# Performance work log

Hardware: AMD Instinct MI355X
Metric: run time of the kernel (lower is better)

## Reference

```python
import jax, jax.numpy as jnp
import numpy as np

B, P, K = 2, 8192, 48
C_IN, C_OUT = 64, 64
N_RADIAL = 8
N_SH = 4            # l=0 (1 component) + l=1 (3 components)
NB = N_RADIAL * N_SH
R_MAX = 2.0
SIGMA = R_MAX / N_RADIAL
EPS = 1e-8


def _edge_basis(rel):
    """Per-edge equivariant basis from relative vectors.
    rel: [..., 3] -> basis [..., NB] = radial Gaussians x (Y_00, Y_1m)."""
    d = jnp.linalg.norm(rel, axis=-1)                              # [...]
    centers = jnp.linspace(0.0, R_MAX, N_RADIAL, dtype=rel.dtype)
    radial = jnp.exp(-0.5 * ((d[..., None] - centers) / SIGMA) ** 2)  # [..., R]
    inv = jnp.where(d > EPS, 1.0 / jnp.maximum(d, EPS), 0.0)
    unit = rel * inv[..., None]                                    # [..., 3]
    sh = jnp.concatenate([jnp.ones_like(d)[..., None], unit], -1)  # [..., 4]
    basis = radial[..., :, None] * sh[..., None, :]                # [..., R, 4]
    return basis.reshape(basis.shape[:-2] + (NB,))


def setup_inputs() -> dict:
    key = jax.random.key(0)
    k1, k2, k3, k4, k5 = jax.random.split(key, 5)
    features = jax.random.normal(k1, (B, C_IN, P), dtype=jnp.float32)
    geometry = jax.random.normal(k2, (B, P, 3), dtype=jnp.float32)
    neighbors = jax.random.randint(k3, (B, P, K), 0, P)
    rel_mask = jax.random.uniform(k4, (B, P, K), dtype=jnp.float32)
    # learned kernel weights: [n_basis, c_out, c_in]
    W = jax.random.normal(k5, (NB, C_OUT, C_IN), dtype=jnp.float32) / np.sqrt(NB * C_IN)
    return {"features": features, "geometry": geometry, "neighbors": neighbors,
            "rel_mask": rel_mask, "W": W}


def reference(features, geometry, neighbors, rel_mask, W):
    # gather neighbor positions: [B, P, K, 3]
    nb_geo = jax.vmap(lambda g, n: g[n])(geometry, neighbors)
    rel = nb_geo - geometry[:, :, None, :]                         # relative vectors
    basis = _edge_basis(rel) * rel_mask[..., None]                 # [B, P, K, NB]
    # gather neighbor features: [B, C_in, P, K]
    nb_feat = jax.vmap(lambda f, n: f[:, n])(features, neighbors)
    # per-edge kernel K_e = sum_n basis_n * W[n] applied to neighbor feats,
    # summed over neighbors -- fused into one contraction (never materialize
    # the [B,P,K,C_out,C_in] kernel tensor):
    out = jnp.einsum('bpkn,ncj,bjpk->bcp', basis, W, nb_feat)
    return out
```

## Files before the change

### kernel.cpp

```cpp
#include <hip/hip_runtime.h>
#include <math.h>

#define B_SZ 2
#define P_SZ 8192
#define K_NB 48
#define NRAD 8
#define NJ 2048
#define PTS 8
#define GSTRIDE 2052
#define EPS_D 1e-8f

__global__ __launch_bounds__(256) void k_transpose(const float* __restrict__ f,
                                                   const float* __restrict__ w,
                                                   float* __restrict__ ft,
                                                   float* __restrict__ wt) {
    __shared__ float tile[64][65];
    int blk = blockIdx.x;
    int t = threadIdx.x;
    if (blk < 256) {
        int b = blk >> 7;
        int p0 = (blk & 127) << 6;
        {
            int pp = t & 63, cq = t >> 6;
#pragma unroll
            for (int i = 0; i < 16; ++i) {
                int c = cq * 16 + i;
                tile[c][pp] = f[((size_t)b * 64 + c) * P_SZ + p0 + pp];
            }
        }
        __syncthreads();
        {
            int cc = t & 63, pq = t >> 6;
#pragma unroll
            for (int i = 0; i < 16; ++i) {
                int p = pq * 16 + i;
                ft[((size_t)b * P_SZ + p0 + p) * 64 + cc] = tile[cc][p];
            }
        }
    } else {
        int n = blk - 256;
        {
            int jj = t & 63, cq = t >> 6;
#pragma unroll
            for (int i = 0; i < 16; ++i) {
                int c = cq * 16 + i;
                tile[c][jj] = w[((size_t)n * 64 + c) * 64 + jj];
            }
        }
        __syncthreads();
        {
            int cc = t & 63, jq = t >> 6;
#pragma unroll
            for (int i = 0; i < 16; ++i) {
                int j = jq * 16 + i;
                wt[((size_t)n * 64 + j) * 64 + cc] = tile[cc][j];
            }
        }
    }
}

__global__ __launch_bounds__(512) void k_main(const float* __restrict__ featT,
                                              const float* __restrict__ geometry,
                                              const int* __restrict__ neighbors,
                                              const float* __restrict__ rel_mask,
                                              const float* __restrict__ Wt,
                                              float* __restrict__ out) {
    __shared__ float G[PTS][GSTRIDE];
    __shared__ float sh_l[PTS][K_NB][4];
    __shared__ float d_l[PTS][K_NB];
    __shared__ int   nbrs_l[PTS][K_NB];

    const int t = threadIdx.x;
    const int blk = blockIdx.x;
    const int b = blk >> 10;
    const int pt0 = (blk & 1023) * PTS;

    if (t < PTS * K_NB) {
        int pt = t / K_NB;
        int k = t - pt * K_NB;
        int p = pt0 + pt;
        size_t base = (size_t)b * P_SZ + p;
        int nb = neighbors[base * K_NB + k];
        const float* gp = &geometry[base * 3];
        const float* gn = &geometry[((size_t)b * P_SZ + nb) * 3];
        float rx = gn[0] - gp[0], ry = gn[1] - gp[1], rz = gn[2] - gp[2];
        float d = sqrtf(rx * rx + ry * ry + rz * rz);
        float mask = rel_mask[base * K_NB + k];
        float inv = (d > EPS_D) ? (1.0f / d) : 0.0f;
        sh_l[pt][k][0] = mask;
        sh_l[pt][k][1] = rx * inv * mask;
        sh_l[pt][k][2] = ry * inv * mask;
        sh_l[pt][k][3] = rz * inv * mask;
        d_l[pt][k] = d;
        nbrs_l[pt][k] = nb;
    }
    __syncthreads();

    {
        const int pt = t >> 6;
        const int ng = (t >> 3) & 7;
        const int jg = t & 7;
        const int j0 = jg * 8;
        const float center = (float)ng * (2.0f / 7.0f);
        float acc[4][8];
#pragma unroll
        for (int s = 0; s < 4; ++s)
#pragma unroll
            for (int j = 0; j < 8; ++j) acc[s][j] = 0.0f;

        const float* fbase = featT + (size_t)b * P_SZ * 64;
#pragma unroll 4
        for (int k = 0; k < K_NB; ++k) {
            int nb = nbrs_l[pt][k];
            const float4* fv = (const float4*)(fbase + (size_t)nb * 64 + j0);
            float4 fA = fv[0];
            float4 fB = fv[1];
            float z = (d_l[pt][k] - center) * 4.0f;
            float rad = __expf(-0.5f * z * z);
            float4 s4 = *(const float4*)&sh_l[pt][k][0];
            float bs[4] = {rad * s4.x, rad * s4.y, rad * s4.z, rad * s4.w};
            float fj[8] = {fA.x, fA.y, fA.z, fA.w, fB.x, fB.y, fB.z, fB.w};
#pragma unroll
            for (int s = 0; s < 4; ++s)
#pragma unroll
                for (int j = 0; j < 8; ++j) acc[s][j] += bs[s] * fj[j];
        }
        const int n0 = ng * 4;
#pragma unroll
        for (int s = 0; s < 4; ++s) {
            *(float4*)&G[pt][(n0 + s) * 64 + j0]     = make_float4(acc[s][0], acc[s][1], acc[s][2], acc[s][3]);
            *(float4*)&G[pt][(n0 + s) * 64 + j0 + 4] = make_float4(acc[s][4], acc[s][5], acc[s][6], acc[s][7]);
        }
    }
    __syncthreads();

    float acc2[8][8];
    {
        const int cg = t & 7;
        const int sg = t >> 3;
        const int c0 = cg * 8;
#pragma unroll
        for (int ci = 0; ci < 8; ++ci)
#pragma unroll
            for (int pt = 0; pt < 8; ++pt) acc2[ci][pt] = 0.0f;

        const int njbase = sg * 32;
        const int rot = (sg * 4) & 31;
#pragma unroll
        for (int it = 0; it < 8; ++it) {
            const int njo = njbase + ((it * 4 + rot) & 31);
            float4 g4[8];
#pragma unroll
            for (int pt = 0; pt < 8; ++pt) g4[pt] = *(const float4*)&G[pt][njo];
            float gf[8][4];
#pragma unroll
            for (int pt = 0; pt < 8; ++pt) {
                gf[pt][0] = g4[pt].x; gf[pt][1] = g4[pt].y;
                gf[pt][2] = g4[pt].z; gf[pt][3] = g4[pt].w;
            }
            float wf[4][8];
#pragma unroll
            for (int q = 0; q < 4; ++q) {
                const float4* wp = (const float4*)(Wt + (size_t)(njo + q) * 64 + c0);
                float4 w0 = wp[0], w1 = wp[1];
                wf[q][0] = w0.x; wf[q][1] = w0.y; wf[q][2] = w0.z; wf[q][3] = w0.w;
                wf[q][4] = w1.x; wf[q][5] = w1.y; wf[q][6] = w1.z; wf[q][7] = w1.w;
            }
#pragma unroll
            for (int q = 0; q < 4; ++q)
#pragma unroll
                for (int ci = 0; ci < 8; ++ci)
#pragma unroll
                    for (int pt = 0; pt < 8; ++pt)
                        acc2[ci][pt] += wf[q][ci] * gf[pt][q];
        }

#pragma unroll
        for (int off = 8; off <= 32; off <<= 1)
#pragma unroll
            for (int ci = 0; ci < 8; ++ci)
#pragma unroll
                for (int pt = 0; pt < 8; ++pt)
                    acc2[ci][pt] += __shfl_xor(acc2[ci][pt], off, 64);
    }
    __syncthreads();

    float* partial = &G[0][0];
    if (((t >> 3) & 7) == 0) {
        const int cg = t & 7;
        const int w = t >> 6;
#pragma unroll
        for (int ci = 0; ci < 8; ++ci) {
            int c = cg * 8 + ci;
            int base = w * 552 + c * 8 + cg * 4;
            *(float4*)&partial[base]     = make_float4(acc2[ci][0], acc2[ci][1], acc2[ci][2], acc2[ci][3]);
            *(float4*)&partial[base + 4] = make_float4(acc2[ci][4], acc2[ci][5], acc2[ci][6], acc2[ci][7]);
        }
    }
    __syncthreads();
    {
        const int c = t >> 3, pt = t & 7;
        const int off = c * 8 + (c >> 3) * 4 + pt;
        float s = 0.0f;
#pragma unroll
        for (int w = 0; w < 8; ++w) s += partial[w * 552 + off];
        out[((size_t)b * 64 + c) * P_SZ + pt0 + pt] = s;
    }
}

extern "C" void kernel_launch(void* const* d_in, const int* in_sizes, int n_in,
                              void* d_out, int out_size, void* d_ws, size_t ws_size,
                              hipStream_t stream) {
    const float* features  = (const float*)d_in[0];
    const float* geometry  = (const float*)d_in[1];
    const int*   neighbors = (const int*)d_in[2];
    const float* rel_mask  = (const float*)d_in[3];
    const float* W         = (const float*)d_in[4];
    float* out = (float*)d_out;

    float* featT = (float*)d_ws;
    float* Wt    = (float*)((char*)d_ws + (size_t)B_SZ * P_SZ * 64 * 4);

    k_transpose<<<288, 256, 0, stream>>>(features, W, featT, Wt);
    k_main<<<B_SZ * (P_SZ / PTS), 512, 0, stream>>>(featT, geometry, neighbors,
                                                    rel_mask, Wt, out);
}
```

Baseline: 218.7 us.

## Stage neighbor feature gathers into LDS with double-buffered async global_load_lds

Replaces the per-thread direct global float4 gathers of neighbor features with wave-level global_load_lds transfers into a double-buffered LDS staging area, 8 neighbors per group. The next group is prefetched while the current one is consumed. The aim is to overlap gather latency with the FMA work and to stop the 8 ng-groups in a wave from loading the same feature row redundantly. In exchange it adds about 32KB of LDS on top of the existing ~66KB, which may reduce occupancy. It also relies on manual vmcnt waits with no barrier, which is correct only because each wave reads just its own staging slice.

```diff
diff --git a/kernel.cpp b/kernel.cpp
--- a/kernel.cpp
+++ b/kernel.cpp
@@ -66,6 +66,7 @@
                                               const float* __restrict__ Wt,
                                               float* __restrict__ out) {
     __shared__ float G[PTS][GSTRIDE];
+    __shared__ float fstage[PTS][2][8][64];
     __shared__ float sh_l[PTS][K_NB][4];
     __shared__ float d_l[PTS][K_NB];
     __shared__ int   nbrs_l[PTS][K_NB];
@@ -98,6 +99,7 @@
 
     {
         const int pt = t >> 6;
+        const int lane = t & 63;
         const int ng = (t >> 3) & 7;
         const int jg = t & 7;
         const int j0 = jg * 8;
@@ -109,21 +111,48 @@
             for (int j = 0; j < 8; ++j) acc[s][j] = 0.0f;
 
         const float* fbase = featT + (size_t)b * P_SZ * 64;
-#pragma unroll 4
-        for (int k = 0; k < K_NB; ++k) {
-            int nb = nbrs_l[pt][k];
-            const float4* fv = (const float4*)(fbase + (size_t)nb * 64 + j0);
-            float4 fA = fv[0];
-            float4 fB = fv[1];
-            float z = (d_l[pt][k] - center) * 4.0f;
-            float rad = __expf(-0.5f * z * z);
-            float4 s4 = *(const float4*)&sh_l[pt][k][0];
-            float bs[4] = {rad * s4.x, rad * s4.y, rad * s4.z, rad * s4.w};
-            float fj[8] = {fA.x, fA.y, fA.z, fA.w, fB.x, fB.y, fB.z, fB.w};
-#pragma unroll
-            for (int s = 0; s < 4; ++s)
-#pragma unroll
-                for (int j = 0; j < 8; ++j) acc[s][j] += bs[s] * fj[j];
+        const int esub = lane >> 4;
+        const int coff = (lane & 15) * 4;
+
+        auto stage = [&](int g, int buf) {
+            int e0 = g * 8 + esub;
+            const float* gs0 = fbase + (size_t)nbrs_l[pt][e0] * 64 + coff;
+            __builtin_amdgcn_global_load_lds(
+                (const __attribute__((address_space(1))) unsigned int*)gs0,
+                (__attribute__((address_space(3))) unsigned int*)&fstage[pt][buf][0][0],
+                16, 0, 0);
+            int e1 = e0 + 4;
+            const float* gs1 = fbase + (size_t)nbrs_l[pt][e1] * 64 + coff;
+            __builtin_amdgcn_global_load_lds(
+                (const __attribute__((address_space(1))) unsigned int*)gs1,
+                (__attribute__((address_space(3))) unsigned int*)&fstage[pt][buf][4][0],
+                16, 0, 0);
+        };
+
+        stage(0, 0);
+        for (int g = 0; g < 6; ++g) {
+            const int buf = g & 1;
+            if (g < 5) {
+                stage(g + 1, buf ^ 1);
+                asm volatile("s_waitcnt vmcnt(2)" ::: "memory");
+            } else {
+                asm volatile("s_waitcnt vmcnt(0)" ::: "memory");
+            }
+#pragma unroll
+            for (int ee = 0; ee < 8; ++ee) {
+                const int e = g * 8 + ee;
+                float z = (d_l[pt][e] - center) * 4.0f;
+                float rad = __expf(-0.5f * z * z);
+                float4 s4 = *(const float4*)&sh_l[pt][e][0];
+                float4 fA = *(const float4*)&fstage[pt][buf][ee][j0];
+                float4 fB = *(const float4*)&fstage[pt][buf][ee][j0 + 4];
+                float bs[4] = {rad * s4.x, rad * s4.y, rad * s4.z, rad * s4.w};
+                float fj[8] = {fA.x, fA.y, fA.z, fA.w, fB.x, fB.y, fB.z, fB.w};
+#pragma unroll
+                for (int s = 0; s < 4; ++s)
+#pragma unroll
+                    for (int j = 0; j < 8; ++j) acc[s][j] += bs[s] * fj[j];
+            }
         }
         const int n0 = ng * 4;
 #pragma unroll
```

Result: faster. 210.1 us (-3.9%).

## Double block size to 1024 threads, halving per-thread work in both stages

Applied to the files above, without the earlier changes.

Moves k_main from 512 to 1024 threads per block. Each thread now covers 4 feature channels instead of 8 in the gather stage and 4 output channels instead of 8 in the W contraction, which cuts register pressure and adds waves for hiding gather latency. The cross-wave reduction is rebuilt for 16 waves with a padded stride-9 layout. In exchange there are more redundant basis/exp computations per edge, more shuffles relative to FMAs, and a larger LDS reduction step.

```diff
diff --git a/kernel.cpp b/kernel.cpp
--- a/kernel.cpp
+++ b/kernel.cpp
@@ -59,12 +59,12 @@
     }
 }
 
-__global__ __launch_bounds__(512) void k_main(const float* __restrict__ featT,
-                                              const float* __restrict__ geometry,
-                                              const int* __restrict__ neighbors,
-                                              const float* __restrict__ rel_mask,
-                                              const float* __restrict__ Wt,
-                                              float* __restrict__ out) {
+__global__ __launch_bounds__(1024) void k_main(const float* __restrict__ featT,
+                                               const float* __restrict__ geometry,
+                                               const int* __restrict__ neighbors,
+                                               const float* __restrict__ rel_mask,
+                                               const float* __restrict__ Wt,
+                                               float* __restrict__ out) {
     __shared__ float G[PTS][GSTRIDE];
     __shared__ float sh_l[PTS][K_NB][4];
     __shared__ float d_l[PTS][K_NB];
@@ -97,50 +97,49 @@
     __syncthreads();
 
     {
-        const int pt = t >> 6;
-        const int ng = (t >> 3) & 7;
-        const int jg = t & 7;
-        const int j0 = jg * 8;
+        const int wave = t >> 6;
+        const int lane = t & 63;
+        const int pt = wave >> 1;
+        const int h  = wave & 1;
+        const int ng = lane >> 3;
+        const int jg = lane & 7;
+        const int j0 = h * 32 + jg * 4;
         const float center = (float)ng * (2.0f / 7.0f);
-        float acc[4][8];
+        float acc[4][4];
 #pragma unroll
         for (int s = 0; s < 4; ++s)
 #pragma unroll
-            for (int j = 0; j < 8; ++j) acc[s][j] = 0.0f;
+            for (int j = 0; j < 4; ++j) acc[s][j] = 0.0f;
 
         const float* fbase = featT + (size_t)b * P_SZ * 64;
 #pragma unroll 4
         for (int k = 0; k < K_NB; ++k) {
             int nb = nbrs_l[pt][k];
-            const float4* fv = (const float4*)(fbase + (size_t)nb * 64 + j0);
-            float4 fA = fv[0];
-            float4 fB = fv[1];
+            float4 fv = *(const float4*)(fbase + (size_t)nb * 64 + j0);
             float z = (d_l[pt][k] - center) * 4.0f;
             float rad = __expf(-0.5f * z * z);
             float4 s4 = *(const float4*)&sh_l[pt][k][0];
             float bs[4] = {rad * s4.x, rad * s4.y, rad * s4.z, rad * s4.w};
-            float fj[8] = {fA.x, fA.y, fA.z, fA.w, fB.x, fB.y, fB.z, fB.w};
+            float fj[4] = {fv.x, fv.y, fv.z, fv.w};
 #pragma unroll
             for (int s = 0; s < 4; ++s)
 #pragma unroll
-                for (int j = 0; j < 8; ++j) acc[s][j] += bs[s] * fj[j];
+                for (int j = 0; j < 4; ++j) acc[s][j] += bs[s] * fj[j];
         }
         const int n0 = ng * 4;
 #pragma unroll
-        for (int s = 0; s < 4; ++s) {
-            *(float4*)&G[pt][(n0 + s) * 64 + j0]     = make_float4(acc[s][0], acc[s][1], acc[s][2], acc[s][3]);
-            *(float4*)&G[pt][(n0 + s) * 64 + j0 + 4] = make_float4(acc[s][4], acc[s][5], acc[s][6], acc[s][7]);
-        }
-    }
-    __syncthreads();
-
-    float acc2[8][8];
+        for (int s = 0; s < 4; ++s)
+            *(float4*)&G[pt][(n0 + s) * 64 + j0] = make_float4(acc[s][0], acc[s][1], acc[s][2], acc[s][3]);
+    }
+    __syncthreads();
+
+    float acc2[4][8];
     {
-        const int cg = t & 7;
-        const int sg = t >> 3;
-        const int c0 = cg * 8;
-#pragma unroll
-        for (int ci = 0; ci < 8; ++ci)
+        const int cg = t & 15;
+        const int sg = t >> 4;
+        const int c0 = cg * 4;
+#pragma unroll
+        for (int ci = 0; ci < 4; ++ci)
 #pragma unroll
             for (int pt = 0; pt < 8; ++pt) acc2[ci][pt] = 0.0f;
 
@@ -158,27 +157,25 @@
                 gf[pt][0] = g4[pt].x; gf[pt][1] = g4[pt].y;
                 gf[pt][2] = g4[pt].z; gf[pt][3] = g4[pt].w;
             }
-            float wf[4][8];
+            float wf[4][4];
 #pragma unroll
             for (int q = 0; q < 4; ++q) {
-                const float4* wp = (const float4*)(Wt + (size_t)(njo + q) * 64 + c0);
-                float4 w0 = wp[0], w1 = wp[1];
+                float4 w0 = *(const float4*)(Wt + (size_t)(njo + q) * 64 + c0);
                 wf[q][0] = w0.x; wf[q][1] = w0.y; wf[q][2] = w0.z; wf[q][3] = w0.w;
-                wf[q][4] = w1.x; wf[q][5] = w1.y; wf[q][6] = w1.z; wf[q][7] = w1.w;
             }
 #pragma unroll
             for (int q = 0; q < 4; ++q)
 #pragma unroll
-                for (int ci = 0; ci < 8; ++ci)
+                for (int ci = 0; ci < 4; ++ci)
 #pragma unroll
                     for (int pt = 0; pt < 8; ++pt)
                         acc2[ci][pt] += wf[q][ci] * gf[pt][q];
         }
 
 #pragma unroll
-        for (int off = 8; off <= 32; off <<= 1)
-#pragma unroll
-            for (int ci = 0; ci < 8; ++ci)
+        for (int off = 16; off <= 32; off <<= 1)
+#pragma unroll
+            for (int ci = 0; ci < 4; ++ci)
 #pragma unroll
                 for (int pt = 0; pt < 8; ++pt)
                     acc2[ci][pt] += __shfl_xor(acc2[ci][pt], off, 64);
@@ -186,24 +183,26 @@
     __syncthreads();
 
     float* partial = &G[0][0];
-    if (((t >> 3) & 7) == 0) {
-        const int cg = t & 7;
-        const int w = t >> 6;
-#pragma unroll
-        for (int ci = 0; ci < 8; ++ci) {
-            int c = cg * 8 + ci;
-            int base = w * 552 + c * 8 + cg * 4;
-            *(float4*)&partial[base]     = make_float4(acc2[ci][0], acc2[ci][1], acc2[ci][2], acc2[ci][3]);
-            *(float4*)&partial[base + 4] = make_float4(acc2[ci][4], acc2[ci][5], acc2[ci][6], acc2[ci][7]);
-        }
-    }
-    __syncthreads();
     {
+        const int lane = t & 63;
+        if (lane < 16) {
+            const int w = t >> 6;
+            const int cg = lane;
+#pragma unroll
+            for (int ci = 0; ci < 4; ++ci) {
+                int c = cg * 4 + ci;
+#pragma unroll
+                for (int pt = 0; pt < 8; ++pt)
+                    partial[w * 576 + c * 9 + pt] = acc2[ci][pt];
+            }
+        }
+    }
+    __syncthreads();
+    if (t < 512) {
         const int c = t >> 3, pt = t & 7;
-        const int off = c * 8 + (c >> 3) * 4 + pt;
         float s = 0.0f;
 #pragma unroll
-        for (int w = 0; w < 8; ++w) s += partial[w * 552 + off];
+        for (int w = 0; w < 16; ++w) s += partial[w * 576 + c * 9 + pt];
         out[((size_t)b * 64 + c) * P_SZ + pt0 + pt] = s;
     }
 }
@@ -222,6 +221,6 @@
     float* Wt    = (float*)((char*)d_ws + (size_t)B_SZ * P_SZ * 64 * 4);
 
     k_transpose<<<288, 256, 0, stream>>>(features, W, featT, Wt);
-    k_main<<<B_SZ * (P_SZ / PTS), 512, 0, stream>>>(featT, geometry, neighbors,
-                                                    rel_mask, Wt, out);
+    k_main<<<B_SZ * (P_SZ / PTS), 1024, 0, stream>>>(featT, geometry, neighbors,
+                                                     rel_mask, Wt, out);
 }
```

New measurement: 226.2 us. 3.4% more time.
